# Kernel optimization log

Hardware: AMD Instinct MI355X
Metric: run time of the kernel (lower is better)

## Reference

```python
import jax, jax.numpy as jnp
import numpy as np
from jax.ops import segment_sum, segment_max

N, D, B = 1536, 32, 8            # nodes, candidate out-degree per node, sequential batch steps
OBS, HID, HEADS, C = 33, 64, 4, 8  # obs_dim, GRU hidden, attn heads, out_dim//heads
E = N * D


def setup_inputs() -> dict:
    key = jax.random.key(0)
    ks = jax.random.split(key, 16)
    g = lambda i, shape, s=0.1: jax.random.normal(ks[i], shape, jnp.float32) * s
    src = jnp.repeat(jnp.arange(N), D)                    # uniform degree -> scatter_topk = row top-k
    dst = jax.random.randint(ks[0], (E,), 0, N)
    return dict(
        H_t=jax.random.normal(ks[1], (B, N, OBS), jnp.float32),
        src=src, dst=dst, k=4,
        W_e1=g(2, (OBS, 32)), b_e1=jnp.zeros(32), W_e2=g(3, (32, 32)), b_e2=jnp.zeros(32),
        ln_g=jnp.ones(32), ln_b=jnp.zeros(32),
        W_ih=g(4, (3 * HID, 32)), W_hh=g(5, (3 * HID, HID)),
        b_ih=jnp.zeros(3 * HID), b_hh=jnp.zeros(3 * HID),
        W_s1=g(6, (2 * HID, 64)), b_s1=jnp.zeros(64), W_s2=g(7, (64, 1)), b_s2=jnp.zeros(1),
        W_gat=g(8, (HID, HEADS * C)), att_src=g(9, (HEADS, C)), att_dst=g(10, (HEADS, C)),
        b_gat=jnp.zeros(HEADS * C),
    )


def _layernorm(x, g, b, eps=1e-5):
    mu = x.mean(-1, keepdims=True)
    var = ((x - mu) ** 2).mean(-1, keepdims=True)
    return (x - mu) * jax.lax.rsqrt(var + eps) * g + b


def _forward(H_t, src, dst, k, W_e1, b_e1, W_e2, b_e2, ln_g, ln_b,
             W_ih, W_hh, b_ih, b_hh, W_s1, b_s1, W_s2, b_s2,
             W_gat, att_src, att_dst, b_gat):
    # ObsEmbedding: Linear-ReLU-Linear-ReLU-LayerNorm, applied to all (B,N) at once
    x = jax.nn.relu(H_t @ W_e1 + b_e1)
    x = jax.nn.relu(x @ W_e2 + b_e2)
    H_emb = _layernorm(x, ln_g, ln_b)              # (B,N,32)

    def step(h, e_t):
        # --- NodeMemory: shared GRUCell, h carried across batch steps ---
        gi = e_t @ W_ih.T + b_ih                   # (N,3H)
        gh = h @ W_hh.T + b_hh
        i_r, i_z, i_n = jnp.split(gi, 3, -1)
        h_r, h_z, h_n = jnp.split(gh, 3, -1)
        r = jax.nn.sigmoid(i_r + h_r)
        z = jax.nn.sigmoid(i_z + h_z)
        n = jnp.tanh(i_n + r * h_n)
        h_new = (1.0 - z) * n + z * h              # (N,HID)

        # --- EdgeScorer: sigmoid MLP score per candidate edge, keep top-k per source ---
        feat = jnp.concatenate([h_new[src], h_new[dst]], -1)        # (E,2*HID)
        score = jax.nn.sigmoid(
            (jax.nn.relu(feat @ W_s1 + b_s1) @ W_s2 + b_s2)[:, 0])  # (E,)
        s2 = score.reshape(N, D)
        top_idx = jax.lax.top_k(s2, k)[1]                           # (N,k)
        keep = (jnp.zeros((N, D), bool)
                .at[jnp.arange(N)[:, None], top_idx].set(True)).reshape(-1)  # (E,)
        w = jnp.where(keep, score, 0.0)                             # soft edge weights

        # --- GATConv (add_self_loops=False), pruned edges masked out of the softmax ---
        xh = (h_new @ W_gat).reshape(N, HEADS, C)
        a_s = (xh * att_src).sum(-1)               # (N,HEADS)
        a_d = (xh * att_dst).sum(-1)
        logit = jax.nn.leaky_relu(a_s[src] + a_d[dst], 0.2)         # (E,HEADS)
        logit = jnp.where(keep[:, None], logit, -1e30)
        m = segment_max(logit, dst, num_segments=N)                 # softmax grouped by target
        ex = jnp.where(keep[:, None], jnp.exp(logit - m[dst]), 0.0)
        ssum = segment_sum(ex, dst, num_segments=N)
        alpha = ex / jnp.clip(ssum[dst], 1e-16)                     # (E,HEADS)

        msg = alpha[:, :, None] * xh[src] * w[:, None, None]        # edge_weight scales messages
        out = segment_sum(msg, dst, num_segments=N).reshape(N, HEADS * C) + b_gat

        # --- densify attention: scatter-accumulate then row-normalize ---
        A = jnp.zeros((HEADS, N, N), alpha.dtype).at[:, src, dst].add(alpha.T)
        A = A / jnp.clip(A.sum(-1, keepdims=True), 1e-9)
        return h_new, (out, A)

    h0 = jnp.zeros((N, HID), H_t.dtype)
    _, (outs, attns) = jax.lax.scan(step, h0, H_emb)
    return outs, attns                              # (B,N,32), (B,HEADS,N,N)


def reference(H_t, src, dst, k, W_e1, b_e1, W_e2, b_e2, ln_g, ln_b,
              W_ih, W_hh, b_ih, b_hh, W_s1, b_s1, W_s2, b_s2,
              W_gat, att_src, att_dst, b_gat):
    return _forward(H_t, src, dst, k, W_e1, b_e1, W_e2, b_e2, ln_g, ln_b,
                    W_ih, W_hh, b_ih, b_hh, W_s1, b_s1, W_s2, b_s2,
                    W_gat, att_src, att_dst, b_gat)
```

## Files before the change

kernel.cpp:

```cpp
#include <hip/hip_runtime.h>
#include <math.h>

#define NN   1536
#define DG   32
#define BB   8
#define OBSD 33
#define HID  64
#define NHEAD 4
#define EE   (NN*DG)
#define MAXDEG 128

__device__ __forceinline__ float sigm(float x){ return 1.0f/(1.0f+expf(-x)); }
__device__ __forceinline__ float rl(float v, int l){
    return __int_as_float(__builtin_amdgcn_readlane(__float_as_int(v), l));
}

__global__ void __launch_bounds__(256) k_embgi(
                      const float* __restrict__ Ht,
                      const float* __restrict__ We1, const float* __restrict__ be1,
                      const float* __restrict__ We2, const float* __restrict__ be2,
                      const float* __restrict__ lng, const float* __restrict__ lnb,
                      const float* __restrict__ Wih, const float* __restrict__ bih,
                      float* __restrict__ GI){
    __shared__ float lwih[192*33];
    int tid = threadIdx.x;
    for(int i=tid;i<192*32;i+=256){ int r=i>>5, c=i&31; lwih[r*33+c]=Wih[i]; }
    __syncthreads();
    int lane = tid & 63;
    int j32 = lane & 31;
    int bn = blockIdx.x*4 + (tid>>6);
    const float* hrow = Ht + (size_t)bn*OBSD;
    float x1 = be1[j32];
    for(int o=0;o<OBSD;o++) x1 += hrow[o]*We1[o*32+j32];
    x1 = fmaxf(x1,0.f);
    float x2 = be2[j32];
    for(int i=0;i<32;i++) x2 += rl(x1,i) * We2[i*32+j32];
    x2 = fmaxf(x2,0.f);
    float mu = x2;
    for(int m=16;m>=1;m>>=1) mu += __shfl_xor(mu, m, 32);
    mu *= (1.0f/32.0f);
    float d = x2-mu; float var = d*d;
    for(int m=16;m>=1;m>>=1) var += __shfl_xor(var, m, 32);
    var *= (1.0f/32.0f);
    float xln = d*rsqrtf(var+1e-5f)*lng[j32]+lnb[j32];
    int j = lane;
    float gr=bih[j], gz=bih[64+j], gn=bih[128+j];
    for(int kk=0;kk<32;kk++){
        float ek = rl(xln, kk);
        gr += ek*lwih[j*33+kk];
        gz += ek*lwih[(64+j)*33+kk];
        gn += ek*lwih[(128+j)*33+kk];
    }
    float* g = GI + (size_t)bn*192;
    g[j]=gr; g[64+j]=gz; g[128+j]=gn;
}

__global__ void k_group(const int* __restrict__ dst, int* __restrict__ cursor,
                        int* __restrict__ gedge){
    int e = blockIdx.x*256+threadIdx.x;
    if(e<EE){
        int d = dst[e];
        int s = atomicAdd(&cursor[d],1);
        if(s<MAXDEG) gedge[d*MAXDEG+s]=e;
    }
}

__global__ void __launch_bounds__(384) k_gru_all(const float* __restrict__ GI,
                       const float* __restrict__ Whh, const float* __restrict__ bhh,
                       float* __restrict__ Hall){
    __shared__ float lw[192*65];
    int tid = threadIdx.x;
    for(int i=tid;i<192*64;i+=384){ int r=i>>6, c=i&63; lw[r*65+c]=Whh[i]; }
    __syncthreads();
    int node = blockIdx.x*6 + (tid>>6);
    int j = tid&63;
    float b_r=bhh[j], b_z=bhh[64+j], b_n=bhh[128+j];
    const float* lwr = lw + j*65;
    const float* lwz = lw + (64+j)*65;
    const float* lwn = lw + (128+j)*65;
    float hold = 0.f;
    for(int t=0;t<BB;t++){
        float hr=b_r, hz=b_z, hn=b_n;
        for(int kk=0;kk<64;kk++){
            float hk = rl(hold,kk);
            hr += hk*lwr[kk];
            hz += hk*lwz[kk];
            hn += hk*lwn[kk];
        }
        const float* g = GI + ((size_t)t*NN+node)*192;
        float r  = sigm(g[j]     + hr);
        float z  = sigm(g[64+j]  + hz);
        float nn_= tanhf(g[128+j] + r*hn);
        hold = (1.f-z)*nn_ + z*hold;
        Hall[((size_t)t*NN+node)*64 + j] = hold;
    }
}

__global__ void __launch_bounds__(256) k_post(const float* __restrict__ Hall,
                       const float* __restrict__ Ws1, const float* __restrict__ Wgat,
                       const float* __restrict__ atts, const float* __restrict__ attd,
                       float* __restrict__ P, float* __restrict__ Q,
                       float* __restrict__ xh, float* __restrict__ as_, float* __restrict__ ad_){
    __shared__ float ws1l[128*64];
    __shared__ float wgl[64*32];
    int tid = threadIdx.x;
    for(int i=tid;i<128*64;i+=256) ws1l[i]=Ws1[i];
    for(int i=tid;i<64*32;i+=256)  wgl[i]=Wgat[i];
    __syncthreads();
    int bn = blockIdx.x*4 + (tid>>6);
    int j = tid&63;
    float hv = Hall[(size_t)bn*64+j];
    float p=0.f,q=0.f,xv=0.f;
    for(int kk=0;kk<64;kk++){
        float hk=rl(hv,kk);
        p += hk*ws1l[kk*64+j];
        q += hk*ws1l[(64+kk)*64+j];
        if(j<32) xv += hk*wgl[kk*32+j];
    }
    P[(size_t)bn*64+j]=p; Q[(size_t)bn*64+j]=q;
    if(j<32){
        xh[(size_t)bn*32+j]=xv;
        float asv = xv*atts[j];
        float adv = xv*attd[j];
        for(int m=1;m<8;m<<=1){ asv += __shfl_xor(asv,m); adv += __shfl_xor(adv,m); }
        if((j&7)==0){ as_[(size_t)bn*4+(j>>3)]=asv; ad_[(size_t)bn*4+(j>>3)]=adv; }
    }
}

__global__ void __launch_bounds__(256) k_edgescore(const float* __restrict__ P, const float* __restrict__ Q,
                       const float* __restrict__ bs1, const float* __restrict__ Ws2,
                       const float* __restrict__ bs2, const int* __restrict__ dst,
                       const int* __restrict__ kptr,
                       const float* __restrict__ as_, const float* __restrict__ ad_,
                       float* __restrict__ rec){
    int t = blockIdx.x;
    int row = blockIdx.y*8 + (threadIdx.x>>5);
    int d = threadIdx.x & 31;
    int e = row*DG + d;
    int de = dst[e];
    const float4* Pr = (const float4*)(P + ((size_t)t*NN+row)*64);
    const float4* Qr = (const float4*)(Q + ((size_t)t*NN+de)*64);
    const float4* B1 = (const float4*)bs1;
    const float4* W2 = (const float4*)Ws2;
    float acc = 0.f;
    #pragma unroll
    for(int jj=0;jj<16;jj++){
        float4 pv=Pr[jj], qv=Qr[jj], bv=B1[jj], wv=W2[jj];
        acc += fmaxf(pv.x+qv.x+bv.x,0.f)*wv.x;
        acc += fmaxf(pv.y+qv.y+bv.y,0.f)*wv.y;
        acc += fmaxf(pv.z+qv.z+bv.z,0.f)*wv.z;
        acc += fmaxf(pv.w+qv.w+bv.w,0.f)*wv.w;
    }
    float score = sigm(acc + bs2[0]);
    int kk = kptr[0]; if(kk>32) kk=32; if(kk<0) kk=0;
    bool sel=false;
    for(int it=0; it<kk; it++){
        float v = sel ? -INFINITY : score;
        int idx = d;
        for(int m=16;m>=1;m>>=1){
            float ov = __shfl_xor(v,m,32);
            int   oi = __shfl_xor(idx,m,32);
            if(ov>v || (ov==v && oi<idx)){ v=ov; idx=oi; }
        }
        if(idx==d) sel=true;
    }
    float wv = sel ? score : 0.f;
    float4 asq = *(const float4*)(as_ + ((size_t)t*NN+row)*4);
    float4 adq = *(const float4*)(ad_ + ((size_t)t*NN+de)*4);
    float ex0,ex1,ex2,ex3;
    {
        float l;
        l = asq.x+adq.x; l = l>0.f ? l : 0.2f*l; ex0 = (wv>0.f)?expf(l):0.f;
        l = asq.y+adq.y; l = l>0.f ? l : 0.2f*l; ex1 = (wv>0.f)?expf(l):0.f;
        l = asq.z+adq.z; l = l>0.f ? l : 0.2f*l; ex2 = (wv>0.f)?expf(l):0.f;
        l = asq.w+adq.w; l = l>0.f ? l : 0.2f*l; ex3 = (wv>0.f)?expf(l):0.f;
    }
    float4* r = (float4*)(rec + ((size_t)t*EE + e)*8);
    r[0] = make_float4(ex0,ex1,ex2,ex3);
    r[1] = make_float4(wv, 0.f, 0.f, 0.f);
}

__global__ void __launch_bounds__(256) k_soft2(const int* __restrict__ gcnt, const int* __restrict__ gedge,
                       const float* __restrict__ rec, const float* __restrict__ xhb,
                       const float* __restrict__ bgat,
                       float* __restrict__ alphab, float* __restrict__ outp){
    int t = blockIdx.x;
    int n = blockIdx.y*4 + (threadIdx.x>>6);
    int lane = threadIdx.x & 63;
    const float* rt   = rec + (size_t)t*EE*8;
    const float* xhbt = xhb + (size_t)t*NN*32;
    float4* alpha     = (float4*)(alphab + (size_t)t*EE*4);
    int cnt = gcnt[n]; if(cnt>MAXDEG) cnt=MAXDEG;
    const int* ge = gedge + (size_t)n*MAXDEG;

    int   e0=0, e1=0;
    float w0=0.f, w1=0.f;
    float4 x0v = make_float4(0,0,0,0), x1v = make_float4(0,0,0,0);
    bool h0v = lane < cnt, h1v = 64+lane < cnt;
    if(h0v){
        e0 = ge[lane];
        const float4* r = (const float4*)(rt + (size_t)e0*8);
        x0v = r[0]; w0 = r[1].x;
    }
    if(h1v){
        e1 = ge[64+lane];
        const float4* r = (const float4*)(rt + (size_t)e1*8);
        x1v = r[0]; w1 = r[1].x;
    }
    float ss[4] = { x0v.x+x1v.x, x0v.y+x1v.y, x0v.z+x1v.z, x0v.w+x1v.w };
    #pragma unroll
    for(int mm=32;mm>=1;mm>>=1){
        #pragma unroll
        for(int h=0;h<4;h++) ss[h] += __shfl_xor(ss[h], mm);
    }
    float inv[4];
    #pragma unroll
    for(int h=0;h<4;h++) inv[h] = 1.0f/fmaxf(ss[h],1e-16f);

    float acc[32];
    #pragma unroll
    for(int c=0;c<32;c++) acc[c]=0.f;

    if(h0v){
        float a0[4] = { x0v.x*inv[0], x0v.y*inv[1], x0v.z*inv[2], x0v.w*inv[3] };
        alpha[e0] = make_float4(a0[0],a0[1],a0[2],a0[3]);
        if(w0>0.f){
            const float4* xr4 = (const float4*)(xhbt + (size_t)(e0>>5)*32);
            #pragma unroll
            for(int h=0;h<4;h++){
                float aw = a0[h]*w0;
                float4 xa = xr4[h*2], xb = xr4[h*2+1];
                acc[h*8+0]+=aw*xa.x; acc[h*8+1]+=aw*xa.y; acc[h*8+2]+=aw*xa.z; acc[h*8+3]+=aw*xa.w;
                acc[h*8+4]+=aw*xb.x; acc[h*8+5]+=aw*xb.y; acc[h*8+6]+=aw*xb.z; acc[h*8+7]+=aw*xb.w;
            }
        }
    }
    if(h1v){
        float a1[4] = { x1v.x*inv[0], x1v.y*inv[1], x1v.z*inv[2], x1v.w*inv[3] };
        alpha[e1] = make_float4(a1[0],a1[1],a1[2],a1[3]);
        if(w1>0.f){
            const float4* xr4 = (const float4*)(xhbt + (size_t)(e1>>5)*32);
            #pragma unroll
            for(int h=0;h<4;h++){
                float aw = a1[h]*w1;
                float4 xa = xr4[h*2], xb = xr4[h*2+1];
                acc[h*8+0]+=aw*xa.x; acc[h*8+1]+=aw*xa.y; acc[h*8+2]+=aw*xa.z; acc[h*8+3]+=aw*xa.w;
                acc[h*8+4]+=aw*xb.x; acc[h*8+5]+=aw*xb.y; acc[h*8+6]+=aw*xb.z; acc[h*8+7]+=aw*xb.w;
            }
        }
    }
    #pragma unroll
    for(int mm=32;mm>=1;mm>>=1){
        #pragma unroll
        for(int c=0;c<32;c++) acc[c] += __shfl_xor(acc[c], mm);
    }
    if(lane==0){
        float4* o = (float4*)(outp + ((size_t)t*NN+n)*32);
        const float4* bg4 = (const float4*)bgat;
        #pragma unroll
        for(int q8=0;q8<8;q8++){
            float4 b = bg4[q8];
            o[q8] = make_float4(acc[q8*4]+b.x, acc[q8*4+1]+b.y, acc[q8*4+2]+b.z, acc[q8*4+3]+b.w);
        }
    }
}

__global__ void __launch_bounds__(256) k_scatter(const float* __restrict__ alphab,
                       const int* __restrict__ dst, float* __restrict__ attn){
    __shared__ float rowbuf[NHEAD][NN];
    __shared__ float rs[NHEAD];
    __shared__ float rsf[NHEAD];
    int t = blockIdx.x;
    int n = blockIdx.y;
    const float* alpha = alphab + (size_t)t*EE*4;
    int tid = threadIdx.x;
    for(int i=tid;i<NHEAD*(NN/4);i+=256) ((float4*)rowbuf)[i]=make_float4(0.f,0.f,0.f,0.f);
    if(tid<NHEAD) rs[tid]=0.f;
    __syncthreads();
    float a=0.f; int de=0; int h=0;
    if(tid<128){
        int d = tid>>2; h = tid&3;
        int e = n*DG+d;
        a = alpha[e*4+h];
        de = dst[e];
        if(a>0.f) atomicAdd(&rs[h], a);
    }
    __syncthreads();
    if(tid<NHEAD) rsf[tid] = 1.0f/fmaxf(rs[tid],1e-9f);
    __syncthreads();
    if(tid<128 && a>0.f) atomicAdd(&rowbuf[h][de], a*rsf[h]);
    __syncthreads();
    size_t tb = (size_t)t*NHEAD*NN*NN;
    for(int i=tid;i<NHEAD*(NN/4);i+=256){
        int hh = i/(NN/4); int c4 = i%(NN/4);
        float4 v = ((const float4*)rowbuf[hh])[c4];
        ((float4*)(attn + tb + (size_t)hh*NN*NN + (size_t)n*NN))[c4] = v;
    }
}

extern "C" void kernel_launch(void* const* d_in, const int* in_sizes, int n_in,
                              void* d_out, int out_size, void* d_ws, size_t ws_size,
                              hipStream_t stream) {
    const float* Ht   = (const float*)d_in[0];
    const int*   src  = (const int*)  d_in[1];
    const int*   dst  = (const int*)  d_in[2];
    const int*   kptr = (const int*)  d_in[3];
    const float* We1  = (const float*)d_in[4];
    const float* be1  = (const float*)d_in[5];
    const float* We2  = (const float*)d_in[6];
    const float* be2  = (const float*)d_in[7];
    const float* lng  = (const float*)d_in[8];
    const float* lnb  = (const float*)d_in[9];
    const float* Wih  = (const float*)d_in[10];
    const float* Whh  = (const float*)d_in[11];
    const float* bih  = (const float*)d_in[12];
    const float* bhh  = (const float*)d_in[13];
    const float* Ws1  = (const float*)d_in[14];
    const float* bs1  = (const float*)d_in[15];
    const float* Ws2  = (const float*)d_in[16];
    const float* bs2  = (const float*)d_in[17];
    const float* Wgat = (const float*)d_in[18];
    const float* atts = (const float*)d_in[19];
    const float* attd = (const float*)d_in[20];
    const float* bgat = (const float*)d_in[21];

    float* outp = (float*)d_out;
    float* attn = outp + (size_t)BB*NN*32;

    float* ws    = (float*)d_ws;
    float* GI    = ws;
    float* Hall  = ws + 2359296;
    float* P     = ws + 3145728;
    float* Q     = ws + 3932160;
    float* xh    = ws + 4718592;
    float* as_   = ws + 5111808;
    float* ad_   = ws + 5160960;
    float* alpha = ws + 5210112;
    float* rec   = ws + 6782976;
    int*   ibase = (int*)(ws + 9928704);
    int*   cursor= ibase;
    int*   gedge = ibase + 2048;

    hipMemsetAsync(cursor, 0, (size_t)NN*sizeof(int), stream);

    k_embgi<<<BB*NN/4, 256, 0, stream>>>(Ht, We1, be1, We2, be2, lng, lnb, Wih, bih, GI);
    k_group<<<EE/256, 256, 0, stream>>>(dst, cursor, gedge);
    k_gru_all<<<NN/6, 384, 0, stream>>>(GI, Whh, bhh, Hall);
    k_post<<<BB*NN/4, 256, 0, stream>>>(Hall, Ws1, Wgat, atts, attd, P, Q, xh, as_, ad_);
    {
        dim3 g(BB, NN/8);
        k_edgescore<<<g, 256, 0, stream>>>(P, Q, bs1, Ws2, bs2, dst, kptr, as_, ad_, rec);
    }
    {
        dim3 gs(BB, NN/4);
        k_soft2<<<gs, 256, 0, stream>>>(cursor, gedge, rec, xh, bgat, alpha, outp);
        dim3 g(BB, NN);
        k_scatter<<<g, 256, 0, stream>>>(alpha, dst, attn);
    }
}
```

Before: 468.7 us.

## Drop per-edge alpha buffer, recompute alpha from per-node sums; fuse grouping into embed kernel

The softmax kernel no longer writes a per-edge alpha array. It stores only per-destination softmax sums, and the scatter kernel recomputes alpha from the stored exp values and those sums. This cuts a large intermediate write and read. The edge-grouping kernel is also folded into the embedding launch as extra blocks, which removes one kernel launch. The cost is extra gather reads of ssum by destination in k_scatter, and the uniform embed launch now carries blocks that return early.

```diff
diff --git a/kernel.cpp b/kernel.cpp
--- a/kernel.cpp
+++ b/kernel.cpp
@@ -9,6 +9,8 @@
 #define NHEAD 4
 #define EE   (NN*DG)
 #define MAXDEG 128
+#define EMB_BLOCKS (BB*NN/4)
+#define GRP_BLOCKS (EE/256)
 
 __device__ __forceinline__ float sigm(float x){ return 1.0f/(1.0f+expf(-x)); }
 __device__ __forceinline__ float rl(float v, int l){
@@ -21,9 +23,20 @@
                       const float* __restrict__ We2, const float* __restrict__ be2,
                       const float* __restrict__ lng, const float* __restrict__ lnb,
                       const float* __restrict__ Wih, const float* __restrict__ bih,
-                      float* __restrict__ GI){
+                      float* __restrict__ GI,
+                      const int* __restrict__ dst, int* __restrict__ cursor,
+                      int* __restrict__ gedge){
     __shared__ float lwih[192*33];
     int tid = threadIdx.x;
+    if(blockIdx.x >= EMB_BLOCKS){
+        int e = (blockIdx.x - EMB_BLOCKS)*256 + tid;
+        if(e<EE){
+            int d = dst[e];
+            int s = atomicAdd(&cursor[d],1);
+            if(s<MAXDEG) gedge[d*MAXDEG+s]=e;
+        }
+        return;
+    }
     for(int i=tid;i<192*32;i+=256){ int r=i>>5, c=i&31; lwih[r*33+c]=Wih[i]; }
     __syncthreads();
     int lane = tid & 63;
@@ -55,16 +68,6 @@
     g[j]=gr; g[64+j]=gz; g[128+j]=gn;
 }
 
-__global__ void k_group(const int* __restrict__ dst, int* __restrict__ cursor,
-                        int* __restrict__ gedge){
-    int e = blockIdx.x*256+threadIdx.x;
-    if(e<EE){
-        int d = dst[e];
-        int s = atomicAdd(&cursor[d],1);
-        if(s<MAXDEG) gedge[d*MAXDEG+s]=e;
-    }
-}
-
 __global__ void __launch_bounds__(384) k_gru_all(const float* __restrict__ GI,
                        const float* __restrict__ Whh, const float* __restrict__ bhh,
                        float* __restrict__ Hall){
@@ -183,13 +186,12 @@
 __global__ void __launch_bounds__(256) k_soft2(const int* __restrict__ gcnt, const int* __restrict__ gedge,
                        const float* __restrict__ rec, const float* __restrict__ xhb,
                        const float* __restrict__ bgat,
-                       float* __restrict__ alphab, float* __restrict__ outp){
+                       float* __restrict__ ssum, float* __restrict__ outp){
     int t = blockIdx.x;
     int n = blockIdx.y*4 + (threadIdx.x>>6);
     int lane = threadIdx.x & 63;
     const float* rt   = rec + (size_t)t*EE*8;
     const float* xhbt = xhb + (size_t)t*NN*32;
-    float4* alpha     = (float4*)(alphab + (size_t)t*EE*4);
     int cnt = gcnt[n]; if(cnt>MAXDEG) cnt=MAXDEG;
     const int* ge = gedge + (size_t)n*MAXDEG;
 
@@ -221,32 +223,26 @@
     #pragma unroll
     for(int c=0;c<32;c++) acc[c]=0.f;
 
-    if(h0v){
+    if(h0v && w0>0.f){
+        const float4* xr4 = (const float4*)(xhbt + (size_t)(e0>>5)*32);
         float a0[4] = { x0v.x*inv[0], x0v.y*inv[1], x0v.z*inv[2], x0v.w*inv[3] };
-        alpha[e0] = make_float4(a0[0],a0[1],a0[2],a0[3]);
-        if(w0>0.f){
-            const float4* xr4 = (const float4*)(xhbt + (size_t)(e0>>5)*32);
-            #pragma unroll
-            for(int h=0;h<4;h++){
-                float aw = a0[h]*w0;
-                float4 xa = xr4[h*2], xb = xr4[h*2+1];
-                acc[h*8+0]+=aw*xa.x; acc[h*8+1]+=aw*xa.y; acc[h*8+2]+=aw*xa.z; acc[h*8+3]+=aw*xa.w;
-                acc[h*8+4]+=aw*xb.x; acc[h*8+5]+=aw*xb.y; acc[h*8+6]+=aw*xb.z; acc[h*8+7]+=aw*xb.w;
-            }
-        }
-    }
-    if(h1v){
+        #pragma unroll
+        for(int h=0;h<4;h++){
+            float aw = a0[h]*w0;
+            float4 xa = xr4[h*2], xb = xr4[h*2+1];
+            acc[h*8+0]+=aw*xa.x; acc[h*8+1]+=aw*xa.y; acc[h*8+2]+=aw*xa.z; acc[h*8+3]+=aw*xa.w;
+            acc[h*8+4]+=aw*xb.x; acc[h*8+5]+=aw*xb.y; acc[h*8+6]+=aw*xb.z; acc[h*8+7]+=aw*xb.w;
+        }
+    }
+    if(h1v && w1>0.f){
+        const float4* xr4 = (const float4*)(xhbt + (size_t)(e1>>5)*32);
         float a1[4] = { x1v.x*inv[0], x1v.y*inv[1], x1v.z*inv[2], x1v.w*inv[3] };
-        alpha[e1] = make_float4(a1[0],a1[1],a1[2],a1[3]);
-        if(w1>0.f){
-            const float4* xr4 = (const float4*)(xhbt + (size_t)(e1>>5)*32);
-            #pragma unroll
-            for(int h=0;h<4;h++){
-                float aw = a1[h]*w1;
-                float4 xa = xr4[h*2], xb = xr4[h*2+1];
-                acc[h*8+0]+=aw*xa.x; acc[h*8+1]+=aw*xa.y; acc[h*8+2]+=aw*xa.z; acc[h*8+3]+=aw*xa.w;
-                acc[h*8+4]+=aw*xb.x; acc[h*8+5]+=aw*xb.y; acc[h*8+6]+=aw*xb.z; acc[h*8+7]+=aw*xb.w;
-            }
+        #pragma unroll
+        for(int h=0;h<4;h++){
+            float aw = a1[h]*w1;
+            float4 xa = xr4[h*2], xb = xr4[h*2+1];
+            acc[h*8+0]+=aw*xa.x; acc[h*8+1]+=aw*xa.y; acc[h*8+2]+=aw*xa.z; acc[h*8+3]+=aw*xa.w;
+            acc[h*8+4]+=aw*xb.x; acc[h*8+5]+=aw*xb.y; acc[h*8+6]+=aw*xb.z; acc[h*8+7]+=aw*xb.w;
         }
     }
     #pragma unroll
@@ -255,6 +251,7 @@
         for(int c=0;c<32;c++) acc[c] += __shfl_xor(acc[c], mm);
     }
     if(lane==0){
+        *(float4*)(ssum + ((size_t)t*NN+n)*4) = make_float4(ss[0],ss[1],ss[2],ss[3]);
         float4* o = (float4*)(outp + ((size_t)t*NN+n)*32);
         const float4* bg4 = (const float4*)bgat;
         #pragma unroll
@@ -265,14 +262,14 @@
     }
 }
 
-__global__ void __launch_bounds__(256) k_scatter(const float* __restrict__ alphab,
+__global__ void __launch_bounds__(256) k_scatter(const float* __restrict__ rec,
+                       const float* __restrict__ ssum,
                        const int* __restrict__ dst, float* __restrict__ attn){
     __shared__ float rowbuf[NHEAD][NN];
     __shared__ float rs[NHEAD];
     __shared__ float rsf[NHEAD];
     int t = blockIdx.x;
     int n = blockIdx.y;
-    const float* alpha = alphab + (size_t)t*EE*4;
     int tid = threadIdx.x;
     for(int i=tid;i<NHEAD*(NN/4);i+=256) ((float4*)rowbuf)[i]=make_float4(0.f,0.f,0.f,0.f);
     if(tid<NHEAD) rs[tid]=0.f;
@@ -281,9 +278,13 @@
     if(tid<128){
         int d = tid>>2; h = tid&3;
         int e = n*DG+d;
-        a = alpha[e*4+h];
+        float ex = rec[((size_t)t*EE + e)*8 + h];
         de = dst[e];
-        if(a>0.f) atomicAdd(&rs[h], a);
+        if(ex>0.f){
+            float ssv = ssum[((size_t)t*NN+de)*4 + h];
+            a = ex / fmaxf(ssv, 1e-16f);
+            atomicAdd(&rs[h], a);
+        }
     }
     __syncthreads();
     if(tid<NHEAD) rsf[tid] = 1.0f/fmaxf(rs[tid],1e-9f);
@@ -323,6 +324,7 @@
     const float* atts = (const float*)d_in[19];
     const float* attd = (const float*)d_in[20];
     const float* bgat = (const float*)d_in[21];
+    (void)src;
 
     float* outp = (float*)d_out;
     float* attn = outp + (size_t)BB*NN*32;
@@ -335,16 +337,16 @@
     float* xh    = ws + 4718592;
     float* as_   = ws + 5111808;
     float* ad_   = ws + 5160960;
-    float* alpha = ws + 5210112;
-    float* rec   = ws + 6782976;
-    int*   ibase = (int*)(ws + 9928704);
+    float* ssum  = ws + 5210112;
+    float* rec   = ws + 5259264;
+    int*   ibase = (int*)(ws + 8404992);
     int*   cursor= ibase;
     int*   gedge = ibase + 2048;
 
     hipMemsetAsync(cursor, 0, (size_t)NN*sizeof(int), stream);
 
-    k_embgi<<<BB*NN/4, 256, 0, stream>>>(Ht, We1, be1, We2, be2, lng, lnb, Wih, bih, GI);
-    k_group<<<EE/256, 256, 0, stream>>>(dst, cursor, gedge);
+    k_embgi<<<EMB_BLOCKS+GRP_BLOCKS, 256, 0, stream>>>(Ht, We1, be1, We2, be2, lng, lnb,
+                                                       Wih, bih, GI, dst, cursor, gedge);
     k_gru_all<<<NN/6, 384, 0, stream>>>(GI, Whh, bhh, Hall);
     k_post<<<BB*NN/4, 256, 0, stream>>>(Hall, Ws1, Wgat, atts, attd, P, Q, xh, as_, ad_);
     {
@@ -353,8 +355,8 @@
     }
     {
         dim3 gs(BB, NN/4);
-        k_soft2<<<gs, 256, 0, stream>>>(cursor, gedge, rec, xh, bgat, alpha, outp);
+        k_soft2<<<gs, 256, 0, stream>>>(cursor, gedge, rec, xh, bgat, ssum, outp);
         dim3 g(BB, NN);
-        k_scatter<<<g, 256, 0, stream>>>(alpha, dst, attn);
-    }
-}
+        k_scatter<<<g, 256, 0, stream>>>(rec, ssum, dst, attn);
+    }
+}
```

After: 465.8 us. Within noise of the previous version (-0.6%).
